# Kernel tuning notes

Hardware: AMD Instinct MI355X
Metric: run time of the kernel (lower is better)

## Reference

```python
import jax, jax.numpy as jnp
import numpy as np

B, S, D = 4, 2048, 1024


def setup_inputs() -> dict:
    key = jax.random.key(0)
    k1, k2, k3, k4 = jax.random.split(key, 4)
    scale = 1.0 / np.sqrt(D)
    return {
        "X_emb": jax.random.normal(k1, (B, S, D), dtype=jnp.float32),
        "W_q": jax.random.normal(k2, (D, D), dtype=jnp.float32) * scale,
        "W_k": jax.random.normal(k3, (D, D), dtype=jnp.float32) * scale,
        "W_v": jax.random.normal(k4, (D, D), dtype=jnp.float32) * scale,
    }


def reference(X_emb, W_q, W_k, W_v):
    # nn.Linear(bias=False): x @ W.T
    Xq = jnp.einsum('bsd,ed->bse', X_emb, W_q)
    Xk = jnp.einsum('bsd,ed->bse', X_emb, W_k)
    Xv = jnp.einsum('bsd,ed->bse', X_emb, W_v)
    S_len = X_emb.shape[-2]
    # scores [B, S, S]; causal mask (strict upper triangle -> -inf)
    att = jnp.einsum('bqe,bke->bqk', Xq, Xk)
    causal = jnp.tril(jnp.ones((S_len, S_len), dtype=bool))
    att = jnp.where(causal, att, -jnp.inf)
    # note: original masks before scaling; -inf / sqrt(d) is still -inf
    att = att / jnp.sqrt(jnp.asarray(Xk.shape[-1], att.dtype))
    w = jax.nn.softmax(att, axis=-1)
    return jnp.einsum('bqk,bke->bqe', w, Xv)
```

## Files before the change

### kernel.cpp

```cpp
#include <hip/hip_runtime.h>
#include <stdint.h>
#include <math.h>

typedef __attribute__((ext_vector_type(8))) __bf16 bf16x8;
typedef __attribute__((ext_vector_type(4))) float f32x4;

__device__ __forceinline__ unsigned short f2bf(float f) {
    unsigned u = __float_as_uint(f);
    u += 0x7FFF + ((u >> 16) & 1);
    return (unsigned short)(u >> 16);
}

__global__ __launch_bounds__(256)
void f32_to_bf16_k(const float* __restrict__ in, unsigned short* __restrict__ out, int n4) {
    int i = blockIdx.x * blockDim.x + threadIdx.x;
    int stride = gridDim.x * blockDim.x;
    for (; i < n4; i += stride) {
        float4 v = reinterpret_cast<const float4*>(in)[i];
        ushort4 o;
        o.x = f2bf(v.x); o.y = f2bf(v.y); o.z = f2bf(v.z); o.w = f2bf(v.w);
        reinterpret_cast<ushort4*>(out)[i] = o;
    }
}

__global__ __launch_bounds__(256)
void w_convert_k(const float* __restrict__ Wq, const float* __restrict__ Wk,
                 const float* __restrict__ Wv, unsigned short* __restrict__ out, int n4) {
    const float* src = blockIdx.y == 0 ? Wq : (blockIdx.y == 1 ? Wk : Wv);
    unsigned short* dst = out + (size_t)blockIdx.y * n4 * 4;
    int i = blockIdx.x * blockDim.x + threadIdx.x;
    int stride = gridDim.x * blockDim.x;
    for (; i < n4; i += stride) {
        float4 v = reinterpret_cast<const float4*>(src)[i];
        ushort4 o;
        o.x = f2bf(v.x); o.y = f2bf(v.y); o.z = f2bf(v.z); o.w = f2bf(v.w);
        reinterpret_cast<ushort4*>(dst)[i] = o;
    }
}

__device__ __forceinline__ void gload16(const unsigned short* g, unsigned short* l) {
    __builtin_amdgcn_global_load_lds(
        (const __attribute__((address_space(1))) unsigned int*)g,
        (__attribute__((address_space(3))) unsigned int*)l, 16, 0, 0);
}

template <typename CT, int MODE>
__global__ __launch_bounds__(256, 2)
void gemm8(const unsigned short* __restrict__ A, const unsigned short* __restrict__ B,
           CT* __restrict__ C, int lda, int ldb, int ldc, int K,
           long long sA, long long sB, long long sC, float scale, int totj)
{
    constexpr int BM = 128, BN = 128;
    constexpr int FM = 4, FN = 4;
    constexpr int ACH = BM * 8;
    constexpr int LPT = (BM + BN) * 8 / 256;

    const int nbx = gridDim.x;
    const int nwg = nbx * gridDim.y;
    const int orig = blockIdx.y * nbx + blockIdx.x;
    const int q8 = nwg >> 3, r8 = nwg & 7;
    const int xcd = orig & 7, idx = orig >> 3;
    const int work = (xcd < r8 ? xcd * (q8 + 1) : r8 * (q8 + 1) + (xcd - r8) * q8) + idx;

    A += (long long)blockIdx.z * sA;
    B += (long long)blockIdx.z * sB;
    C += (long long)blockIdx.z * sC;

    __shared__ unsigned short As[2][BM * 64];
    __shared__ unsigned short Bs[2][BN * 64];

    const int t    = threadIdx.x;
    const int lane = t & 63;
    const int wid  = t >> 6;
    const int wm   = wid >> 1, wn = wid & 1;
    const int rsel = lane & 15;
    const int gsel = lane >> 4;

    auto stage = [&](int buf, int kt, int m0, int n0) {
        const int k0 = kt * 64;
#pragma unroll
        for (int i = 0; i < LPT; ++i) {
            int ci = i * 256 + t;
            if (ci < ACH) {
                int row = ci >> 3, cc = ci & 7;
                gload16(A + (long long)(m0 + row) * lda + k0 + ((cc ^ (row & 7)) * 8),
                        &As[buf][ci * 8]);
            } else {
                int cj = ci - ACH;
                int row = cj >> 3, cc = cj & 7;
                gload16(B + (long long)(n0 + row) * ldb + k0 + ((cc ^ (row & 7)) * 8),
                        &Bs[buf][cj * 8]);
            }
        }
    };

    auto run_tile = [&](int br, int bc, int kmax, bool first) {
        const int m0 = br * BM, n0 = bc * BN;
        f32x4 acc[FM][FN];
#pragma unroll
        for (int m = 0; m < FM; ++m)
#pragma unroll
            for (int n = 0; n < FN; ++n) acc[m][n] = (f32x4){0.f, 0.f, 0.f, 0.f};

        const int nk = kmax >> 6;
        if (!first) {
            __builtin_amdgcn_s_barrier();
            __builtin_amdgcn_sched_barrier(0);
        }
        stage(0, 0, m0, n0);

        for (int kt = 0; kt < nk; ++kt) {
            const int c = kt & 1;
            __builtin_amdgcn_s_barrier();
            __builtin_amdgcn_sched_barrier(0);
            if (kt + 1 < nk) {
                stage(c ^ 1, kt + 1, m0, n0);
                asm volatile("s_waitcnt vmcnt(8)" ::: "memory");
            } else {
                asm volatile("s_waitcnt vmcnt(0)" ::: "memory");
            }
            __builtin_amdgcn_s_barrier();
            __builtin_amdgcn_sched_barrier(0);

            bf16x8 aF[FM][2], bF[FN][2];
#pragma unroll
            for (int m = 0; m < FM; ++m)
#pragma unroll
                for (int ks = 0; ks < 2; ++ks) {
                    int r  = wm * (FM * 16) + m * 16 + rsel;
                    int cc = ks * 4 + gsel;
                    aF[m][ks] = *reinterpret_cast<const bf16x8*>(
                        &As[c][r * 64 + ((cc ^ (r & 7)) * 8)]);
                }
#pragma unroll
            for (int n = 0; n < FN; ++n)
#pragma unroll
                for (int ks = 0; ks < 2; ++ks) {
                    int rb = wn * (FN * 16) + n * 16 + rsel;
                    int cc = ks * 4 + gsel;
                    bF[n][ks] = *reinterpret_cast<const bf16x8*>(
                        &Bs[c][rb * 64 + ((cc ^ (rb & 7)) * 8)]);
                }

            __builtin_amdgcn_s_setprio(1);
#pragma unroll
            for (int m = 0; m < FM; ++m)
#pragma unroll
                for (int n = 0; n < FN; ++n)
#pragma unroll
                    for (int ks = 0; ks < 2; ++ks)
                        acc[m][n] = __builtin_amdgcn_mfma_f32_16x16x32_bf16(
                            aF[m][ks], bF[n][ks], acc[m][n], 0, 0, 0);
            __builtin_amdgcn_s_setprio(0);
        }

        const int rowl = gsel * 4;
#pragma unroll
        for (int m = 0; m < FM; ++m) {
#pragma unroll
            for (int n = 0; n < FN; ++n) {
#pragma unroll
                for (int i = 0; i < 4; ++i) {
                    int r  = m0 + wm * (FM * 16) + m * 16 + rowl + i;
                    int cI = n0 + wn * (FN * 16) + n * 16 + rsel;
                    float v = acc[m][n][i] * scale;
                    if constexpr (sizeof(CT) == 2)
                        ((unsigned short*)C)[(long long)r * ldc + cI] = f2bf(v);
                    else
                        ((float*)C)[(long long)r * ldc + cI] = v;
                }
            }
        }
    };

    auto tri = [&](int w, int& br, int& bc) {
        int rr = (int)((sqrtf(8.0f * (float)w + 1.0f) - 1.0f) * 0.5f);
        while ((rr + 1) * (rr + 2) / 2 <= w) ++rr;
        while (rr * (rr + 1) / 2 > w) --rr;
        br = rr; bc = w - rr * (rr + 1) / 2;
    };

    if constexpr (MODE == 0) {
        run_tile(work / nbx, work % nbx, K, true);
    } else if constexpr (MODE == 1) {
        int br, bc;
        tri(work, br, bc);
        run_tile(br, bc, K, true);
        const int e = work >> 4;
        if ((work & 15) == 8 && nwg + e < totj) {
            tri(nwg + e, br, bc);
            run_tile(br, bc, K, false);
        }
    } else {
        const int p = work / nbx, bc = work % nbx;
        run_tile(p, bc, (p + 1) * BM, true);
        run_tile(totj - 1 - p, bc, (totj - p) * BM, false);
    }
}

__device__ __forceinline__ float waveMax(float v) {
#pragma unroll
    for (int o = 32; o > 0; o >>= 1) v = fmaxf(v, __shfl_xor(v, o, 64));
    return v;
}
__device__ __forceinline__ float waveSum(float v) {
#pragma unroll
    for (int o = 32; o > 0; o >>= 1) v += __shfl_xor(v, o, 64);
    return v;
}

__global__ __launch_bounds__(256)
void softmax_causal(const float* __restrict__ S, unsigned short* __restrict__ P, int Slen) {
    __shared__ float e[2048];
    __shared__ float red[4];
    long long row = blockIdx.x;
    int q = (int)(row % Slen);
    const float* srow = S + row * (long long)Slen;
    unsigned short* prow = P + row * (long long)Slen;
    int len = q + 1;
    int t = threadIdx.x;

    int nfull = len >> 2;
    float mx = -3.0e38f;
    for (int i = t; i < nfull; i += 256) {
        float4 v = reinterpret_cast<const float4*>(srow)[i];
        e[4 * i + 0] = v.x; e[4 * i + 1] = v.y;
        e[4 * i + 2] = v.z; e[4 * i + 3] = v.w;
        mx = fmaxf(fmaxf(fmaxf(mx, v.x), v.y), fmaxf(v.z, v.w));
    }
    if (t < (len & 3)) {
        float v = srow[nfull * 4 + t];
        e[nfull * 4 + t] = v;
        mx = fmaxf(mx, v);
    }
    mx = waveMax(mx);
    if ((t & 63) == 0) red[t >> 6] = mx;
    __syncthreads();
    mx = fmaxf(fmaxf(red[0], red[1]), fmaxf(red[2], red[3]));

    float sum = 0.f;
    for (int k = t; k < len; k += 256) {
        float v = __expf(e[k] - mx);
        e[k] = v;
        sum += v;
    }
    sum = waveSum(sum);
    __syncthreads();
    if ((t & 63) == 0) red[t >> 6] = sum;
    __syncthreads();
    sum = red[0] + red[1] + red[2] + red[3];
    float inv = 1.0f / sum;

    int wlim = ((q >> 7) + 1) << 7;
    __syncthreads();
    for (int i = t; i < (wlim >> 2); i += 256) {
        int k = 4 * i;
        ushort4 o;
        o.x = (k + 0 < len) ? f2bf(e[k + 0] * inv) : (unsigned short)0;
        o.y = (k + 1 < len) ? f2bf(e[k + 1] * inv) : (unsigned short)0;
        o.z = (k + 2 < len) ? f2bf(e[k + 2] * inv) : (unsigned short)0;
        o.w = (k + 3 < len) ? f2bf(e[k + 3] * inv) : (unsigned short)0;
        reinterpret_cast<ushort4*>(prow)[i] = o;
    }
}

extern "C" void kernel_launch(void* const* d_in, const int* in_sizes, int n_in,
                              void* d_out, int out_size, void* d_ws, size_t ws_size,
                              hipStream_t stream) {
    const int B = 4, S = 2048, D = 1024;
    const float* X  = (const float*)d_in[0];
    const float* Wq = (const float*)d_in[1];
    const float* Wk = (const float*)d_in[2];
    const float* Wv = (const float*)d_in[3];
    float* out = (float*)d_out;

    char* ws = (char*)d_ws;
    unsigned short* Xb  = (unsigned short*)ws; ws += (size_t)B * S * D * 2;
    unsigned short* Wqb = (unsigned short*)ws; ws += (size_t)D * D * 2;
    unsigned short* Wkb = (unsigned short*)ws; ws += (size_t)D * D * 2;
    unsigned short* Wvb = (unsigned short*)ws; ws += (size_t)D * D * 2;
    unsigned short* Qb  = (unsigned short*)ws; ws += (size_t)B * S * D * 2;
    unsigned short* Kb  = (unsigned short*)ws; ws += (size_t)B * S * D * 2;
    unsigned short* Vt  = (unsigned short*)ws; ws += (size_t)B * S * D * 2;
    float*          Sc  = (float*)ws;          ws += (size_t)B * S * S * 4;
    unsigned short* P   = (unsigned short*)ws; ws += (size_t)B * S * S * 2;

    f32_to_bf16_k<<<2048, 256, 0, stream>>>(X, Xb, B * S * D / 4);
    w_convert_k<<<dim3(512, 3), 256, 0, stream>>>(Wq, Wk, Wv, Wqb, D * D / 4);

    dim3 blk(256);
    gemm8<unsigned short, 0><<<dim3(D / 128, B * S / 128, 2), blk, 0, stream>>>(
        Xb, Wqb, Qb, D, D, D, D, 0, (long long)D * D, (long long)B * S * D, 1.0f, 0);

    gemm8<unsigned short, 0><<<dim3(S / 128, D / 128, B), blk, 0, stream>>>(
        Wvb, Xb, Vt, D, D, S, D, 0, (long long)S * D, (long long)D * S, 1.0f, 0);

    gemm8<float, 1><<<dim3(8, 16, B), blk, 0, stream>>>(
        Qb, Kb, Sc, D, D, S, D, (long long)S * D, (long long)S * D, (long long)S * S,
        0.03125f, 136);

    softmax_causal<<<B * S, 256, 0, stream>>>(Sc, P, S);

    gemm8<float, 2><<<dim3(D / 128, 8, B), blk, 0, stream>>>(
        P, Vt, out, S, S, D, S, (long long)S * S, (long long)D * S, (long long)S * D,
        1.0f, 16);
}
```

Baseline: 178.9 us.

## Precompute staging pointers and launch one tile per block for P@V

The GEMM staging loop now precomputes per-thread global pointers with the swizzle folded in and advances them by 64 each k-step. This replaces the per-iteration row/column index arithmetic and the A/B branch. The P@V GEMM no longer pairs a short and a long causal row tile in one block. It now launches twice as many blocks, each running a single tile, with an interleaved short/long ordering across workgroups. This raises parallelism but leaves per-block work unbalanced, so the hardware scheduler has to even out the load.

```diff
diff --git a/kernel.cpp b/kernel.cpp
--- a/kernel.cpp
+++ b/kernel.cpp
@@ -52,8 +52,6 @@
 {
     constexpr int BM = 128, BN = 128;
     constexpr int FM = 4, FN = 4;
-    constexpr int ACH = BM * 8;
-    constexpr int LPT = (BM + BN) * 8 / 256;
 
     const int nbx = gridDim.x;
     const int nwg = nbx * gridDim.y;
@@ -75,24 +73,8 @@
     const int wm   = wid >> 1, wn = wid & 1;
     const int rsel = lane & 15;
     const int gsel = lane >> 4;
-
-    auto stage = [&](int buf, int kt, int m0, int n0) {
-        const int k0 = kt * 64;
-#pragma unroll
-        for (int i = 0; i < LPT; ++i) {
-            int ci = i * 256 + t;
-            if (ci < ACH) {
-                int row = ci >> 3, cc = ci & 7;
-                gload16(A + (long long)(m0 + row) * lda + k0 + ((cc ^ (row & 7)) * 8),
-                        &As[buf][ci * 8]);
-            } else {
-                int cj = ci - ACH;
-                int row = cj >> 3, cc = cj & 7;
-                gload16(B + (long long)(n0 + row) * ldb + k0 + ((cc ^ (row & 7)) * 8),
-                        &Bs[buf][cj * 8]);
-            }
-        }
-    };
+    const int srow = t >> 3;
+    const int swz  = ((t & 7) ^ (srow & 7)) * 8;
 
     auto run_tile = [&](int br, int bc, int kmax, bool first) {
         const int m0 = br * BM, n0 = bc * BN;
@@ -101,20 +83,39 @@
         for (int m = 0; m < FM; ++m)
 #pragma unroll
             for (int n = 0; n < FN; ++n) acc[m][n] = (f32x4){0.f, 0.f, 0.f, 0.f};
+
+        const unsigned short* gpA[4];
+        const unsigned short* gpB[4];
+#pragma unroll
+        for (int i = 0; i < 4; ++i) {
+            gpA[i] = A + (long long)(m0 + srow + 32 * i) * lda + swz;
+            gpB[i] = B + (long long)(n0 + srow + 32 * i) * ldb + swz;
+        }
+
+        auto stage = [&](int buf) {
+#pragma unroll
+            for (int i = 0; i < 4; ++i)
+                gload16(gpA[i], &As[buf][i * 2048 + t * 8]);
+#pragma unroll
+            for (int i = 0; i < 4; ++i)
+                gload16(gpB[i], &Bs[buf][i * 2048 + t * 8]);
+#pragma unroll
+            for (int i = 0; i < 4; ++i) { gpA[i] += 64; gpB[i] += 64; }
+        };
 
         const int nk = kmax >> 6;
         if (!first) {
             __builtin_amdgcn_s_barrier();
             __builtin_amdgcn_sched_barrier(0);
         }
-        stage(0, 0, m0, n0);
+        stage(0);
 
         for (int kt = 0; kt < nk; ++kt) {
             const int c = kt & 1;
             __builtin_amdgcn_s_barrier();
             __builtin_amdgcn_sched_barrier(0);
             if (kt + 1 < nk) {
-                stage(c ^ 1, kt + 1, m0, n0);
+                stage(c ^ 1);
                 asm volatile("s_waitcnt vmcnt(8)" ::: "memory");
             } else {
                 asm volatile("s_waitcnt vmcnt(0)" ::: "memory");
@@ -192,9 +193,10 @@
             run_tile(br, bc, K, false);
         }
     } else {
-        const int p = work / nbx, bc = work % nbx;
-        run_tile(p, bc, (p + 1) * BM, true);
-        run_tile(totj - 1 - p, bc, (totj - p) * BM, false);
+        const int s = work & 1, pp = work >> 1;
+        const int col = pp & 7, rp = pp >> 3;
+        const int row = s ? 15 - rp : rp;
+        run_tile(row, col, (row + 1) * BM, true);
     }
 }
 
@@ -301,7 +303,7 @@
 
     softmax_causal<<<B * S, 256, 0, stream>>>(Sc, P, S);
 
-    gemm8<float, 2><<<dim3(D / 128, 8, B), blk, 0, stream>>>(
+    gemm8<float, 3><<<dim3(8, 16, B), blk, 0, stream>>>(
         P, Vt, out, S, S, D, S, (long long)S * S, (long long)D * S, (long long)S * D,
-        1.0f, 16);
-}
+        1.0f, 0);
+}
```

Result: no change. 176.1 us (-1.6%).
